# Optimization experiments

Measured on AMD Instinct MI355X. Metric: run time of the kernel, lower is better.

The kernel has to match this reference:

```python
import jax, jax.numpy as jnp
import numpy as np

EPS = 1e-6


def setup_inputs() -> dict:
    key = jax.random.key(0)
    k1, k2, k3, k4, k5 = jax.random.split(key, 5)
    B, L, K, NFG, NH, NFO = 4, 1024, 32, 4, 16, 32
    return {
        "beta": jax.random.normal(k1, (B, L, NFG * NH), dtype=jnp.float32),
        "self_attention": jax.random.normal(k2, (B, L, NFG * NH), dtype=jnp.float32),
        "attn_coef": jax.random.normal(k3, (B, L, K, NFG * NH), dtype=jnp.float32),
        "node_out": jax.random.normal(k4, (B, L, K, NFO * NH), dtype=jnp.float32),
        "graph_weights": jax.random.uniform(k5, (B, L, K, NFG), dtype=jnp.float32),
    }


def reference(beta, self_attention, attn_coef, node_out, graph_weights):
    B, L, K, nfg = graph_weights.shape
    nh = attn_coef.shape[-1] // nfg
    nfo = node_out.shape[-1] // nh

    beta = beta.reshape(B, L, nfg, nh)
    sa = self_attention.reshape(B, L, nfg, nh)
    ac = attn_coef.reshape(B, L, K, nfg, nh)
    no = node_out.reshape(B, L, K, nfo, nh)

    # add self-attention term to the first (self) neighbor slot
    ac = ac.at[:, :, 0].add(sa)
    # beta gating, broadcast over neighbors
    ac = ac * (beta[:, :, None] + EPS)
    # stabilized exp over (K, nfg) jointly
    ac = ac - jnp.max(ac, axis=(-3, -2), keepdims=True)
    weighted = jnp.exp(ac) * graph_weights[..., None]          # [B,L,K,nfg,nh]
    attn_final = jnp.sum(weighted, axis=-2)                    # [B,L,K,nh]
    attn_final = attn_final / (jnp.sum(jnp.abs(attn_final), axis=-2, keepdims=True) + EPS)
    # weighted aggregation over neighbors
    output = jnp.einsum("blkfh,blkh->blfh", no, attn_final).reshape(B, L, nfo * nh)
    return output, attn_final
```

## Files before the change

kernel.cpp:

```cpp
#include <hip/hip_runtime.h>

#define EPS 1e-6f

constexpr int KNB = 32;
constexpr int NFG = 4;
constexpr int NH  = 16;
constexpr int NFO = 32;
constexpr int FH  = NFG * NH;
constexpr int ACN = KNB * FH;
constexpr int ON  = NFO * NH;
constexpr int KN  = KNB * NH;

__global__ __launch_bounds__(256, 4)
void attn_fused(const float* __restrict__ beta,
                const float* __restrict__ sa,
                const float* __restrict__ ac,
                const float* __restrict__ no,
                const float* __restrict__ gw,
                float* __restrict__ out,
                float* __restrict__ attn_out)
{
    const int bl   = blockIdx.x;
    const int tid  = threadIdx.x;
    const int lane = tid & 63;
    const int wv   = tid >> 6;

    __shared__ float s_ac[ACN];
    __shared__ float s_attn[KN];
    __shared__ float s_gw[KNB * NFG];
    __shared__ float s_bg[FH];
    __shared__ float s_wm[4 * NH];
    __shared__ float s_wd[4 * NH];
    __shared__ float s_part[ON];

    const size_t blz = (size_t)bl;
    const float* acp = ac + blz * ACN;
    const float* nop = no + blz * (size_t)(KNB * ON);

    if (tid < FH)        s_bg[tid] = beta[blz * FH + tid] + EPS;
    if (tid < KNB * NFG) s_gw[tid] = gw[blz * (KNB * NFG) + tid];
    __syncthreads();

    const int h = tid & 15;

    float lmax = -INFINITY;
    #pragma unroll
    for (int j = 0; j < 8; ++j) {
        const int idx = tid + j * 256;
        float v = acp[idx];
        if (j == 0 && tid < FH) v += sa[blz * FH + tid];
        v *= s_bg[idx & 63];
        s_ac[idx] = v;
        lmax = fmaxf(lmax, v);
    }

    lmax = fmaxf(lmax, __shfl_xor(lmax, 16, 64));
    lmax = fmaxf(lmax, __shfl_xor(lmax, 32, 64));
    if (lane < 16) s_wm[wv * 16 + lane] = lmax;
    __syncthreads();
    const float m = fmaxf(fmaxf(s_wm[h], s_wm[16 + h]),
                          fmaxf(s_wm[32 + h], s_wm[48 + h]));

    const int k0 = tid >> 4;
    float a0 = 0.f, a1 = 0.f;
    #pragma unroll
    for (int f = 0; f < NFG; ++f) {
        a0 += __expf(s_ac[k0 * 64 + f * 16 + h] - m)        * s_gw[k0 * 4 + f];
        a1 += __expf(s_ac[(k0 + 16) * 64 + f * 16 + h] - m) * s_gw[(k0 + 16) * 4 + f];
    }

    float ls = fabsf(a0) + fabsf(a1);
    ls += __shfl_xor(ls, 16, 64);
    ls += __shfl_xor(ls, 32, 64);
    if (lane < 16) s_wd[wv * 16 + lane] = ls;
    __syncthreads();
    const float den = s_wd[h] + s_wd[16 + h] + s_wd[32 + h] + s_wd[48 + h] + EPS;

    const float n0 = a0 / den;
    const float n1 = a1 / den;
    s_attn[tid]       = n0;
    s_attn[tid + 256] = n1;
    attn_out[blz * KN + tid]       = n0;
    attn_out[blz * KN + tid + 256] = n1;
    __syncthreads();

    const int half = tid >> 7;
    const int u    = tid & 127;
    const int p    = u * 4;
    const float* basep = nop + half * ON + p;
    float4 acc = make_float4(0.f, 0.f, 0.f, 0.f);
    #pragma unroll 8
    for (int j = 0; j < 16; ++j) {
        const float4 v = *reinterpret_cast<const float4*>(basep + j * 1024);
        const float4 w = *reinterpret_cast<const float4*>(
            &s_attn[(2 * j + half) * 16 + (p & 15)]);
        acc.x += v.x * w.x;
        acc.y += v.y * w.y;
        acc.z += v.z * w.z;
        acc.w += v.w * w.w;
    }
    if (half) {
        *reinterpret_cast<float4*>(&s_part[p]) = acc;
    }
    __syncthreads();
    if (!half) {
        const float4 q = *reinterpret_cast<const float4*>(&s_part[p]);
        acc.x += q.x; acc.y += q.y; acc.z += q.z; acc.w += q.w;
        *reinterpret_cast<float4*>(out + blz * ON + p) = acc;
    }
}

extern "C" void kernel_launch(void* const* d_in, const int* in_sizes, int n_in,
                              void* d_out, int out_size, void* d_ws, size_t ws_size,
                              hipStream_t stream) {
    const float* beta = (const float*)d_in[0];
    const float* sa   = (const float*)d_in[1];
    const float* ac   = (const float*)d_in[2];
    const float* no   = (const float*)d_in[3];
    const float* gw   = (const float*)d_in[4];

    const int BL = in_sizes[0] / FH;
    float* out      = (float*)d_out;
    float* attn_out = out + (size_t)BL * ON;

    attn_fused<<<BL, 256, 0, stream>>>(beta, sa, ac, no, gw, out, attn_out);
}
```

Baseline: 387.2 us.

## Split fused kernel into attention-weight kernel and separate einsum kernel

The single fused kernel is split in two. The first computes the normalized attention weights and writes them to global memory. The second handles two rows per block, reads those weights back and streams node_out over all 32 neighbors per thread, so the shared-memory partial-sum reduction goes away. This lets each kernel use its own occupancy settings, but adds a second launch and a global round trip for the weights, and loses any overlap between the two phases.

```diff
diff --git a/kernel.cpp b/kernel.cpp
--- a/kernel.cpp
+++ b/kernel.cpp
@@ -10,15 +10,14 @@
 constexpr int ACN = KNB * FH;
 constexpr int ON  = NFO * NH;
 constexpr int KN  = KNB * NH;
+constexpr int ROWSTRIDE = KNB * ON;
 
 __global__ __launch_bounds__(256, 4)
-void attn_fused(const float* __restrict__ beta,
-                const float* __restrict__ sa,
-                const float* __restrict__ ac,
-                const float* __restrict__ no,
-                const float* __restrict__ gw,
-                float* __restrict__ out,
-                float* __restrict__ attn_out)
+void attn_weights(const float* __restrict__ beta,
+                  const float* __restrict__ sa,
+                  const float* __restrict__ ac,
+                  const float* __restrict__ gw,
+                  float* __restrict__ attn_out)
 {
     const int bl   = blockIdx.x;
     const int tid  = threadIdx.x;
@@ -26,16 +25,13 @@
     const int wv   = tid >> 6;
 
     __shared__ float s_ac[ACN];
-    __shared__ float s_attn[KN];
     __shared__ float s_gw[KNB * NFG];
     __shared__ float s_bg[FH];
     __shared__ float s_wm[4 * NH];
     __shared__ float s_wd[4 * NH];
-    __shared__ float s_part[ON];
 
     const size_t blz = (size_t)bl;
     const float* acp = ac + blz * ACN;
-    const float* nop = no + blz * (size_t)(KNB * ON);
 
     if (tid < FH)        s_bg[tid] = beta[blz * FH + tid] + EPS;
     if (tid < KNB * NFG) s_gw[tid] = gw[blz * (KNB * NFG) + tid];
@@ -76,38 +72,41 @@
     __syncthreads();
     const float den = s_wd[h] + s_wd[16 + h] + s_wd[32 + h] + s_wd[48 + h] + EPS;
 
-    const float n0 = a0 / den;
-    const float n1 = a1 / den;
-    s_attn[tid]       = n0;
-    s_attn[tid + 256] = n1;
-    attn_out[blz * KN + tid]       = n0;
-    attn_out[blz * KN + tid + 256] = n1;
+    attn_out[blz * KN + tid]       = a0 / den;
+    attn_out[blz * KN + tid + 256] = a1 / den;
+}
+
+__global__ __launch_bounds__(256, 8)
+void einsum_k(const float* __restrict__ no,
+              const float* __restrict__ attn,
+              float* __restrict__ out)
+{
+    const int tid = threadIdx.x;
+    const int r   = tid >> 7;
+    const int u   = tid & 127;
+    const int p   = u * 4;
+    const int row = blockIdx.x * 2 + r;
+
+    __shared__ float s_attn[2 * KN];
+
+    *reinterpret_cast<float4*>(&s_attn[r * KN + p]) =
+        *reinterpret_cast<const float4*>(attn + (size_t)row * KN + p);
     __syncthreads();
 
-    const int half = tid >> 7;
-    const int u    = tid & 127;
-    const int p    = u * 4;
-    const float* basep = nop + half * ON + p;
+    const float*  basep = no + (size_t)row * ROWSTRIDE + p;
+    const float*  wbase = &s_attn[r * KN + (p & 15)];
+
     float4 acc = make_float4(0.f, 0.f, 0.f, 0.f);
-    #pragma unroll 8
-    for (int j = 0; j < 16; ++j) {
-        const float4 v = *reinterpret_cast<const float4*>(basep + j * 1024);
-        const float4 w = *reinterpret_cast<const float4*>(
-            &s_attn[(2 * j + half) * 16 + (p & 15)]);
+    #pragma unroll 4
+    for (int k = 0; k < KNB; ++k) {
+        const float4 v = *reinterpret_cast<const float4*>(basep + k * ON);
+        const float4 w = *reinterpret_cast<const float4*>(wbase + k * NH);
         acc.x += v.x * w.x;
         acc.y += v.y * w.y;
         acc.z += v.z * w.z;
         acc.w += v.w * w.w;
     }
-    if (half) {
-        *reinterpret_cast<float4*>(&s_part[p]) = acc;
-    }
-    __syncthreads();
-    if (!half) {
-        const float4 q = *reinterpret_cast<const float4*>(&s_part[p]);
-        acc.x += q.x; acc.y += q.y; acc.z += q.z; acc.w += q.w;
-        *reinterpret_cast<float4*>(out + blz * ON + p) = acc;
-    }
+    *reinterpret_cast<float4*>(out + (size_t)row * ON + p) = acc;
 }
 
 extern "C" void kernel_launch(void* const* d_in, const int* in_sizes, int n_in,
@@ -123,5 +122,6 @@
     float* out      = (float*)d_out;
     float* attn_out = out + (size_t)BL * ON;
 
-    attn_fused<<<BL, 256, 0, stream>>>(beta, sa, ac, no, gw, out, attn_out);
+    attn_weights<<<BL, 256, 0, stream>>>(beta, sa, ac, gw, attn_out);
+    einsum_k<<<BL / 2, 256, 0, stream>>>(no, attn_out, out);
 }
```

Result: no change. 390.7 us (+0.9%).
